# Kernel optimization log

Hardware: AMD Instinct MI355X
Metric: run time of the kernel (lower is better)

Reference implementation:

```python
import jax, jax.numpy as jnp
import numpy as np

DIM = 1024
HEADS = 16
BIAS_INIT = 5.0
POST_LOG_SCALE = 1.0


def setup_inputs() -> dict:
    key = jax.random.key(0)
    kx, kw = jax.random.split(key)
    x = jax.random.normal(kx, (2, 2048, DIM), dtype=jnp.float32)
    # nn.Linear(dim, heads): weight [heads, dim], bias initialized to bias_init
    W = jax.random.normal(kw, (HEADS, DIM), dtype=jnp.float32) * (1.0 / np.sqrt(DIM))
    b = jnp.full((HEADS,), BIAS_INIT, dtype=jnp.float32)
    return {"x": x, "W": W, "b": b}


def reference(x, W, b):
    # linear -> [b, n, h], rearrange to [b, h, n], logsigmoid, scale
    logits = jnp.einsum('bnd,hd->bhn', x, W) + b[None, :, None]
    fg = jax.nn.log_sigmoid(logits) * POST_LOG_SCALE
    # cumulative sum over sequence
    fg = jnp.cumsum(fg, axis=-1)
    # pairwise subtract: bias[b,h,i,j] = fg[b,h,i] - fg[b,h,j] (causal case)
    return fg[:, :, :, None] - fg[:, :, None, :]
```

## Files before the change

### kernel.cpp

```cpp
#include <hip/hip_runtime.h>
#include <hip/hip_bf16.h>

#define DIM   1024
#define HEADS 16
#define B     2
#define N     2048

typedef float f32x4 __attribute__((ext_vector_type(4)));

__global__ __launch_bounds__(256) void logits_kernel(
    const float* __restrict__ x, const float* __restrict__ W,
    const float* __restrict__ bias, float* __restrict__ logits) {
  const int bn   = blockIdx.x;
  const int tid  = threadIdx.x;
  const int wave = tid >> 6;
  const int lane = tid & 63;

  const f32x4* xrow = (const f32x4*)(x + (size_t)bn * DIM);
  f32x4 xv[4];
#pragma unroll
  for (int k = 0; k < 4; ++k) xv[k] = xrow[lane * 4 + k];

#pragma unroll
  for (int hh = 0; hh < 4; ++hh) {
    const int h = wave * 4 + hh;
    const f32x4* wrow = (const f32x4*)(W + (size_t)h * DIM);
    float s = 0.0f;
#pragma unroll
    for (int k = 0; k < 4; ++k) {
      f32x4 wv = wrow[lane * 4 + k];
      s += wv.x * xv[k].x + wv.y * xv[k].y + wv.z * xv[k].z + wv.w * xv[k].w;
    }
#pragma unroll
    for (int off = 32; off > 0; off >>= 1) s += __shfl_down(s, off, 64);
    if (lane == 0) {
      const int b = bn >> 11;
      const int n = bn & (N - 1);
      logits[((size_t)(b * HEADS + h)) * N + n] = s + bias[h];
    }
  }
}

__device__ __forceinline__ float logsig(float z) {
  return fminf(z, 0.0f) - log1pf(__expf(-fabsf(z)));
}

__global__ __launch_bounds__(256) void cumsum_kernel(
    const float* __restrict__ logits, float* __restrict__ fg) {
  const int bh  = blockIdx.x;
  const int tid = threadIdx.x;
  const float* lp = logits + (size_t)bh * N;
  float*       fp = fg     + (size_t)bh * N;

  f32x4 a = ((const f32x4*)lp)[tid * 2];
  f32x4 c = ((const f32x4*)lp)[tid * 2 + 1];
  float v[8] = {a.x, a.y, a.z, a.w, c.x, c.y, c.z, c.w};

  float run = 0.0f;
#pragma unroll
  for (int i = 0; i < 8; ++i) { v[i] = logsig(v[i]); run += v[i]; v[i] = run; }
  const float total = run;

  const int lane = tid & 63, wv = tid >> 6;
  float sc = total;
#pragma unroll
  for (int off = 1; off < 64; off <<= 1) {
    float t = __shfl_up(sc, off, 64);
    if (lane >= off) sc += t;
  }

  __shared__ float wtot[4];
  if (lane == 63) wtot[wv] = sc;
  __syncthreads();
  float wofs = 0.0f;
  for (int w = 0; w < wv; ++w) wofs += wtot[w];

  const float base = wofs + sc - total;
  f32x4 o0 = {base + v[0], base + v[1], base + v[2], base + v[3]};
  f32x4 o1 = {base + v[4], base + v[5], base + v[6], base + v[7]};
  ((f32x4*)fp)[tid * 2]     = o0;
  ((f32x4*)fp)[tid * 2 + 1] = o1;
}

__global__ __launch_bounds__(256) void outer_kernel(
    const float* __restrict__ fg, float* __restrict__ out) {
  const int row = blockIdx.x;
  const int bh  = row >> 11;
  const int i   = row & (N - 1);
  const float fi = fg[(size_t)bh * N + i];
  const f32x4* fj = (const f32x4*)(fg + (size_t)bh * N);
  f32x4* o = (f32x4*)(out + (size_t)row * N);
  const int tid = threadIdx.x;
#pragma unroll
  for (int k = 0; k < 2; ++k) {
    const int idx = tid + k * 256;
    f32x4 v = fj[idx];
    f32x4 r = {fi - v.x, fi - v.y, fi - v.z, fi - v.w};
    __builtin_nontemporal_store(r, &o[idx]);
  }
}

extern "C" void kernel_launch(void* const* d_in, const int* in_sizes, int n_in,
                              void* d_out, int out_size, void* d_ws, size_t ws_size,
                              hipStream_t stream) {
  const float* x    = (const float*)d_in[0];
  const float* W    = (const float*)d_in[1];
  const float* bias = (const float*)d_in[2];
  float* out = (float*)d_out;

  float* logits = (float*)d_ws;
  float* fg     = logits + (size_t)B * HEADS * N;

  logits_kernel<<<B * N, 256, 0, stream>>>(x, W, bias, logits);
  cumsum_kernel<<<B * HEADS, 256, 0, stream>>>(logits, fg);
  outer_kernel<<<B * HEADS * N, 256, 0, stream>>>(fg, out);
}
```

Measured before the change: 122.0 us.

## Have each wave write eight output rows, reusing the loaded fg row

The outer-difference kernel now assigns eight consecutive output rows to each wave instead of one row per 256-thread block. Each wave loads the full fg row into registers once, reads its eight fi values with two vector loads, and writes all eight rows. This cuts redundant fg loads and the block count, so per-block launch overhead drops. It also replaces nontemporal stores with ordinary stores, which may change cache behaviour on the 512 MB output write.

```diff
diff --git a/kernel.cpp b/kernel.cpp
--- a/kernel.cpp
+++ b/kernel.cpp
@@ -5,6 +5,7 @@
 #define HEADS 16
 #define B     2
 #define N     2048
+#define RPW   8
 
 typedef float f32x4 __attribute__((ext_vector_type(4)));
 
@@ -84,19 +85,36 @@
 
 __global__ __launch_bounds__(256) void outer_kernel(
     const float* __restrict__ fg, float* __restrict__ out) {
-  const int row = blockIdx.x;
-  const int bh  = row >> 11;
-  const int i   = row & (N - 1);
-  const float fi = fg[(size_t)bh * N + i];
-  const f32x4* fj = (const f32x4*)(fg + (size_t)bh * N);
-  f32x4* o = (f32x4*)(out + (size_t)row * N);
-  const int tid = threadIdx.x;
+  const int tid  = threadIdx.x;
+  const int wave = tid >> 6;
+  const int lane = tid & 63;
+  const int gw   = blockIdx.x * 4 + wave;
+  const int row0 = gw * RPW;
+  const int bh   = row0 >> 11;
+  const int i0   = row0 & (N - 1);
+
+  const float* frow = fg + ((size_t)bh << 11);
+
+  const f32x4* fj = (const f32x4*)frow;
+  f32x4 vj[8];
 #pragma unroll
-  for (int k = 0; k < 2; ++k) {
-    const int idx = tid + k * 256;
-    f32x4 v = fj[idx];
-    f32x4 r = {fi - v.x, fi - v.y, fi - v.z, fi - v.w};
-    __builtin_nontemporal_store(r, &o[idx]);
+  for (int k = 0; k < 8; ++k) vj[k] = fj[lane + k * 64];
+
+  f32x4 fia = *(const f32x4*)(frow + i0);
+  f32x4 fib = *(const f32x4*)(frow + i0 + 4);
+  const float fi[RPW] = {fia.x, fia.y, fia.z, fia.w, fib.x, fib.y, fib.z, fib.w};
+
+  f32x4* orow = (f32x4*)(out + ((size_t)row0 << 11));
+#pragma unroll
+  for (int r = 0; r < RPW; ++r) {
+    const float f = fi[r];
+#pragma unroll
+    for (int k = 0; k < 8; ++k) {
+      f32x4 v = vj[k];
+      f32x4 s = {f - v.x, f - v.y, f - v.z, f - v.w};
+      orow[lane + k * 64] = s;
+    }
+    orow += N / 4;
   }
 }
 
@@ -113,5 +131,5 @@
 
   logits_kernel<<<B * N, 256, 0, stream>>>(x, W, bias, logits);
   cumsum_kernel<<<B * HEADS, 256, 0, stream>>>(logits, fg);
-  outer_kernel<<<B * HEADS * N, 256, 0, stream>>>(fg, out);
+  outer_kernel<<<B * HEADS * N / (RPW * 4), 256, 0, stream>>>(fg, out);
 }
```

Result: no change. 123.4 us (+1.1%).
